# Performance work log

Measured on AMD Instinct MI355X. Metric: run time of the kernel, lower is better.

## Reference

```python
import jax, jax.numpy as jnp
import numpy as np

NUM_CLASSES = 7
CLASS_WEIGHT = 1.0
BOX_WEIGHT = 1.0


def _linear_sum_assignment(cost):
    """Exact Hungarian via shortest augmenting paths (Jonker-Volgenant style).
    Matches scipy.optimize.linear_sum_assignment for rectangular matrices:
    returns (row_ind, col_ind) of length min(n, m), row_ind sorted ascending."""
    C = np.asarray(cost, dtype=np.float64)
    transposed = C.shape[0] > C.shape[1]
    if transposed:
        C = C.T
    n, m = C.shape  # n <= m
    u = np.zeros(n + 1)
    v = np.zeros(m + 1)
    p = np.zeros(m + 1, dtype=np.int64)    # p[j]: row matched to col j (1-based); 0 = free
    way = np.zeros(m + 1, dtype=np.int64)
    for i in range(1, n + 1):
        p[0] = i
        j0 = 0
        minv = np.full(m + 1, np.inf)
        used = np.zeros(m + 1, dtype=bool)
        while True:
            used[j0] = True
            i0 = p[j0]
            cur = C[i0 - 1] - u[i0] - v[1:]
            free = ~used[1:]
            better = free & (cur < minv[1:])
            minv[1:][better] = cur[better]
            way[1:][better] = j0
            masked = np.where(free, minv[1:], np.inf)
            j0n = int(np.argmin(masked)) + 1
            delta = masked[j0n - 1]
            uj = np.nonzero(used)[0]
            u[p[uj]] += delta
            v[uj] -= delta
            minv[1:][free] -= delta
            j0 = j0n
            if p[j0] == 0:
                break
        while j0 != 0:   # augment along alternating path
            j1 = way[j0]
            p[j0] = p[j1]
            j0 = j1
    cols = np.nonzero(p[1:] > 0)[0]
    rows = p[1:][cols] - 1
    if transposed:
        rows, cols = cols, rows
    order = np.argsort(rows)
    return rows[order], cols[order]


def _cost_matrices(pred_logits, pred_boxes, gt_labels, gt_boxes):
    """Batched cost: class_weight * (-log_softmax gathered at gt labels) + box_weight * L1 cdist on xyz."""
    B, Q, _ = pred_logits.shape
    M = gt_labels.shape[1]
    log_probs = jax.nn.log_softmax(pred_logits, axis=-1)                       # (B,Q,C)
    idx = jnp.broadcast_to(gt_labels[:, None, :], (B, Q, M))
    class_cost = -jnp.take_along_axis(log_probs, idx, axis=2)                  # (B,Q,M)
    box_cost = jnp.sum(jnp.abs(pred_boxes[:, :, None, :3] - gt_boxes[:, None, :, :3]), axis=-1)  # (B,Q,M)
    return CLASS_WEIGHT * class_cost + BOX_WEIGHT * box_cost


def _matched_loss(pred_logits, pred_boxes, gt_labels, gt_boxes, rows, cols):
    B = pred_logits.shape[0]
    bidx = jnp.arange(B)[:, None]
    ml = pred_logits[bidx, rows]          # (B,M,C) matched logits
    mb = pred_boxes[bidx, rows]           # (B,M,7) matched boxes
    gl = gt_labels[bidx, cols]            # (B,M)
    gb = gt_boxes[bidx, cols]             # (B,M,7)
    logp = jax.nn.log_softmax(ml, axis=-1)
    ce = -jnp.mean(jnp.take_along_axis(logp, gl[..., None], axis=-1)[..., 0], axis=1)  # (B,)
    l1 = jnp.mean(jnp.abs(mb - gb), axis=(1, 2))                                       # (B,)
    return jnp.mean(CLASS_WEIGHT * ce + BOX_WEIGHT * l1)


def setup_inputs() -> dict:
    key = jax.random.key(0)
    k1, k2, k3, k4 = jax.random.split(key, 4)
    B, Q, M = 128, 900, 100
    return {
        'pred_logits': jax.random.normal(k1, (B, Q, NUM_CLASSES), dtype=jnp.float32),
        'pred_boxes': jax.random.normal(k2, (B, Q, 7), dtype=jnp.float32),
        'gt_labels': jax.random.randint(k3, (B, M), 0, NUM_CLASSES, dtype=jnp.int32),
        'gt_boxes': jax.random.normal(k4, (B, M, 7), dtype=jnp.float32),
    }


def reference(pred_logits, pred_boxes, gt_labels, gt_boxes):
    B = pred_logits.shape[0]
    M = gt_labels.shape[1]
    # Assignment is done on detached costs (host-side), matching the original module.
    cost = np.asarray(_cost_matrices(pred_logits, pred_boxes, gt_labels, gt_boxes))
    rows = np.zeros((B, M), dtype=np.int64)
    cols = np.zeros((B, M), dtype=np.int64)
    for b in range(B):
        r, c = _linear_sum_assignment(cost[b])
        rows[b], cols[b] = r, c
    return _matched_loss(pred_logits, pred_boxes, gt_labels, gt_boxes,
                         jnp.asarray(rows), jnp.asarray(cols))
```

## Files before the change

kernel.cpp:

```cpp
#include <hip/hip_runtime.h>
#include <math.h>


#define NQ   900
#define NG   100
#define NC   7
#define CPL  15
#define ROUNDS 10
#define INFF __builtin_inff()

__device__ __forceinline__ float readlane_f(float x, int l) {
  return __int_as_float(__builtin_amdgcn_readlane(__float_as_int(x), l));
}
template<int CTRL>
__device__ __forceinline__ float dpp_min_step(float x) {
  int y = __builtin_amdgcn_update_dpp(__float_as_int(x), __float_as_int(x),
                                      CTRL, 0xf, 0xf, false);
  return fminf(x, __int_as_float(y));
}
__device__ __forceinline__ float wave_min_b(float x) {
  x = dpp_min_step<0x111>(x);
  x = dpp_min_step<0x112>(x);
  x = dpp_min_step<0x114>(x);
  x = dpp_min_step<0x118>(x);
  x = dpp_min_step<0x142>(x);
  x = dpp_min_step<0x143>(x);
  return __int_as_float(__builtin_amdgcn_readlane(__float_as_int(x), 63));
}
template<int CTRL>
__device__ __forceinline__ void dpp_min2_step(float &a, float &b) {
  const int INFI = 0x7f800000;
  float a2 = __int_as_float(__builtin_amdgcn_update_dpp(
      INFI, __float_as_int(a), CTRL, 0xf, 0xf, false));
  float b2 = __int_as_float(__builtin_amdgcn_update_dpp(
      INFI, __float_as_int(b), CTRL, 0xf, 0xf, false));
  float lo = fminf(a, a2);
  float hi = fmaxf(a, a2);
  b = fminf(hi, fminf(b, b2));
  a = lo;
}
__device__ __forceinline__ void wave_min2_b(float m1, float m2,
                                            float &o1, float &o2) {
  dpp_min2_step<0x111>(m1, m2);
  dpp_min2_step<0x112>(m1, m2);
  dpp_min2_step<0x114>(m1, m2);
  dpp_min2_step<0x118>(m1, m2);
  dpp_min2_step<0x142>(m1, m2);
  dpp_min2_step<0x143>(m1, m2);
  o1 = readlane_f(m1, 63);
  o2 = readlane_f(m2, 63);
}
template<int CTRL>
__device__ __forceinline__ float dpp_add_step(float x) {
  int y = __builtin_amdgcn_update_dpp(0, __float_as_int(x),
                                      CTRL, 0xf, 0xf, true);
  return x + __int_as_float(y);
}
__device__ __forceinline__ float wave_sum_b(float x) {
  x = dpp_add_step<0x111>(x);
  x = dpp_add_step<0x112>(x);
  x = dpp_add_step<0x114>(x);
  x = dpp_add_step<0x118>(x);
  x = dpp_add_step<0x142>(x);
  x = dpp_add_step<0x143>(x);
  return __int_as_float(__builtin_amdgcn_readlane(__float_as_int(x), 63));
}
__device__ __forceinline__ void gl_lds16(const float* g, float* lds_base) {
  __builtin_amdgcn_global_load_lds(
      (const __attribute__((address_space(1))) unsigned int*)g,
      (__attribute__((address_space(3))) unsigned int*)lds_base, 16, 0, 0);
}
__device__ __forceinline__ float sel7v(float a0,float a1,float a2,float a3,
                                       float a4,float a5,float a6,int lab){
  float r = a0;
  r = lab==1 ? a1 : r;  r = lab==2 ? a2 : r;  r = lab==3 ? a3 : r;
  r = lab==4 ? a4 : r;  r = lab==5 ? a5 : r;  r = lab==6 ? a6 : r;
  return r;
}

__global__ __launch_bounds__(256, 1) void hungarian_fused_kernel(
    const float* __restrict__ logits, const float* __restrict__ pboxes,
    const int* __restrict__ glabels, const float* __restrict__ gboxes,
    float* __restrict__ out, float inv_B)
{
  const int b = blockIdx.x, tid = threadIdx.x;
  const int lane = tid & 63, w = tid >> 6;

  __shared__ __align__(16) float s_raw[NQ * NC];
  __shared__ __align__(16) float s_nlpT[NC * 1024];
  __shared__ __align__(16) float s_pb[960 * NC];
  __shared__ __align__(16) float s_gb[NG * NC];
  __shared__ __align__(16) int   s_glab[NG];
  __shared__ float s_u[NG + 1];
  __shared__ float s_v[CPL * 64];
  __shared__ int   s_p[NQ];
  __shared__ unsigned s_bid[NQ];
  __shared__ int   s_rmatch[NG];
  __shared__ float s_bm1[NG], s_bm2[NG];
  __shared__ int   s_bc[NG];
  __shared__ unsigned long long s_fm[2];
  __shared__ float s_f1v[NG]; __shared__ int s_f1c[NG];
  __shared__ float s_f2v[NG]; __shared__ int s_f2c[NG];
  __shared__ int   s_mlist[128];

  {
    const float* Lg = logits + (size_t)b * NQ * NC;
    const float* Pg = pboxes + (size_t)b * NQ * NC;
    const float* Gg = gboxes + (size_t)b * NG * NC;
    const int*   Bg = glabels + (size_t)b * NG;
    #pragma unroll
    for (int t = 0; t < 7; t++) {
      int i = (t << 8) + tid;
      if (i < (NQ * NC) / 4) {
        gl_lds16(Lg + i * 4, s_raw + ((t << 8) + (w << 6)) * 4);
        gl_lds16(Pg + i * 4, s_pb  + ((t << 8) + (w << 6)) * 4);
      }
    }
    if (tid < (NG * NC) / 4) gl_lds16(Gg + tid * 4, s_gb + (w << 6) * 4);
    if (tid < NG / 4) gl_lds16((const float*)Bg + tid * 4, (float*)s_glab);
    for (int i = tid; i < (960 - NQ) * NC; i += 256) s_pb[NQ * NC + i] = 0.f;
    for (int c = tid; c < NQ; c += 256) { s_p[c] = 0x7fffffff; s_bid[c] = 0xFFFFFFFFu; }
    for (int i = tid; i < CPL * 64; i += 256) s_v[i] = 0.f;
    if (tid == 0) s_u[0] = 0.f;
  }
  __syncthreads();

  for (int i = tid; i < 960; i += 256) {
    int L = i & 63, t = i >> 6;
    int q = L * CPL + t;
    float o[NC];
    if (q < NQ) {
      float x[NC];
      #pragma unroll
      for (int c = 0; c < NC; c++) x[c] = s_raw[q * NC + c];
      float mx = x[0];
      #pragma unroll
      for (int c = 1; c < NC; c++) mx = fmaxf(mx, x[c]);
      float tt[NC]; float se = 0.f;
      #pragma unroll
      for (int c = 0; c < NC; c++) { tt[c] = x[c] - mx; se += __expf(tt[c]); }
      float lg = __logf(se);
      #pragma unroll
      for (int c = 0; c < NC; c++) o[c] = lg - tt[c];
    } else {
      #pragma unroll
      for (int c = 0; c < NC; c++) o[c] = INFF;
    }
    #pragma unroll
    for (int c = 0; c < NC; c++) s_nlpT[c * 1024 + t * 64 + L] = o[c];
  }
  __syncthreads();

  const bool lval = (lane < NQ / CPL);
  float cpx[CPL], cpy[CPL], cpz[CPL];
  #pragma unroll
  for (int t = 0; t < CPL; t++) {
    int c = lane * CPL + t;
    cpx[t]=s_pb[c*NC+0]; cpy[t]=s_pb[c*NC+1]; cpz[t]=s_pb[c*NC+2];
  }

  for (int rl = 0; rl < 25; rl++) {
    int r = w * 25 + rl;
    int lab = s_glab[r];
    float gx = s_gb[r*NC+0], gy = s_gb[r*NC+1], gz = s_gb[r*NC+2];
    float m1 = INFF; int c1t = 0;
    #pragma unroll
    for (int t = 0; t < CPL; t++) {
      float nl = s_nlpT[lab*1024 + t*64 + lane];
      float bs = fabsf(cpx[t]-gx)+fabsf(cpy[t]-gy)+fabsf(cpz[t]-gz);
      float cost = nl + bs;
      bool lt1 = cost < m1;
      c1t = lt1 ? t : c1t;
      m1 = fminf(m1, cost);
    }
    float w1 = wave_min_b(m1);
    unsigned long long mk = __ballot(m1 == w1);
    int src = (int)__builtin_ctzll(mk);
    int col = __builtin_amdgcn_readlane(lane * CPL + c1t, src);
    if (lane == 0) {
      s_u[r + 1] = w1;
      s_bc[r] = col;
      atomicMin(&s_p[col], r + 1);
    }
  }
  __syncthreads();
  for (int c = tid; c < NQ; c += 256) if (s_p[c] == 0x7fffffff) s_p[c] = 0;
  if (tid < NG) {
    int c = s_bc[tid];
    s_rmatch[tid] = (s_p[c] == tid + 1) ? c + 1 : 0;
  }
  __syncthreads();

  for (int round = 0; round < ROUNDS; round++) {
    if (w == 0) {
      unsigned long long m = __ballot(s_rmatch[lane] == 0);
      if (lane == 0) s_fm[0] = m;
    } else if (w == 1) {
      unsigned long long m = __ballot((lane < NG - 64) && s_rmatch[64 + lane] == 0);
      if (lane == 0) s_fm[1] = m;
    }
    __syncthreads();
    const unsigned long long fm0r = s_fm[0], fm1r = s_fm[1];
    if ((fm0r | fm1r) == 0) break;
    float vreg[CPL];
    #pragma unroll
    for (int t = 0; t < CPL; t++) vreg[t] = s_v[t*64 + lane];
    {
      unsigned long long mm0 = fm0r, mm1 = fm1r;
      int idx = 0;
      while (mm0 | mm1) {
        int r;
        if (mm0) { int b2 = (int)__builtin_ctzll(mm0); mm0 &= mm0 - 1; r = b2; }
        else     { int b2 = (int)__builtin_ctzll(mm1); mm1 &= mm1 - 1; r = 64 + b2; }
        if ((idx++ & 3) != w) continue;
        int lab = s_glab[r];
        float gx = s_gb[r*NC+0], gy = s_gb[r*NC+1], gz = s_gb[r*NC+2];
        float m1 = INFF, m2 = INFF; int c1t = 0;
        #pragma unroll
        for (int t = 0; t < CPL; t++) {
          float nl = s_nlpT[lab*1024 + t*64 + lane];
          float bs = fabsf(cpx[t]-gx)+fabsf(cpy[t]-gy)+fabsf(cpz[t]-gz);
          float cost = (nl + bs) - vreg[t];
          bool lt1 = cost < m1;
          m2 = lt1 ? m1 : fminf(m2, cost);
          c1t = lt1 ? t : c1t;
          m1 = fminf(m1, cost);
        }
        float w1, w2;
        wave_min2_b(m1, m2, w1, w2);
        unsigned long long mk = __ballot(m1 == w1);
        int src = (int)__builtin_ctzll(mk);
        int col1 = __builtin_amdgcn_readlane(lane * CPL + c1t, src);
        if (lane == 0) {
          s_bm1[r] = w1; s_bm2[r] = w2; s_bc[r] = col1;
          atomicMin(&s_bid[col1],
                    (__float_as_uint(w1) & 0xFFFFFF80u) | (unsigned)(r + 1));
        }
      }
    }
    __syncthreads();
    if (tid < NG) {
      bool wasfree = (tid < 64) ? ((fm0r >> tid) & 1ull)
                                : ((fm1r >> (tid - 64)) & 1ull);
      if (wasfree) {
        int c = s_bc[tid];
        if ((s_bid[c] & 0x7Fu) == (unsigned)(tid + 1)) {
          int dold = s_p[c];
          s_p[c] = tid + 1;
          s_rmatch[tid] = c + 1;
          if (dold > 0) s_rmatch[dold - 1] = 0;
          s_u[tid + 1] = s_bm2[tid];
          s_v[(c % CPL) * 64 + (c / CPL)] -= (s_bm2[tid] - s_bm1[tid]);
        }
      }
    }
    __syncthreads();
    if (tid < NG) {
      bool wasfree = (tid < 64) ? ((fm0r >> tid) & 1ull)
                                : ((fm1r >> (tid - 64)) & 1ull);
      if (wasfree) s_bid[s_bc[tid]] = 0xFFFFFFFFu;
    }
  }
  __syncthreads();

  if (w == 0) {
    unsigned long long m = __ballot(s_rmatch[lane] == 0);
    if (lane == 0) s_fm[0] = m;
  } else if (w == 1) {
    unsigned long long m = __ballot((lane < NG - 64) && s_rmatch[64 + lane] == 0);
    if (lane == 0) s_fm[1] = m;
  }
  __syncthreads();
  const unsigned long long ff0 = s_fm[0], ff1 = s_fm[1];
  const int nfinal = __popcll(ff0) + __popcll(ff1);
  if (nfinal > 0) {
    float vreg[CPL];
    #pragma unroll
    for (int t = 0; t < CPL; t++) vreg[t] = s_v[t*64 + lane];
    unsigned long long mm0 = ff0, mm1 = ff1;
    int idx = 0;
    while (mm0 | mm1) {
      int r;
      if (mm0) { int b2 = (int)__builtin_ctzll(mm0); mm0 &= mm0 - 1; r = b2; }
      else     { int b2 = (int)__builtin_ctzll(mm1); mm1 &= mm1 - 1; r = 64 + b2; }
      if ((idx++ & 3) != w) continue;
      int lab = s_glab[r];
      float gx = s_gb[r*NC+0], gy = s_gb[r*NC+1], gz = s_gb[r*NC+2];
      float m1 = INFF;
      #pragma unroll
      for (int t = 0; t < CPL; t++) {
        float nl = s_nlpT[lab*1024 + t*64 + lane];
        float bs = fabsf(cpx[t]-gx)+fabsf(cpy[t]-gy)+fabsf(cpz[t]-gz);
        m1 = fminf(m1, (nl + bs) - vreg[t]);
      }
      float w1 = wave_min_b(m1);
      if (lane == 0) s_u[r + 1] = w1;
    }
    __syncthreads();
  }

  if (nfinal > 0) {
  unsigned fmask = 0;
  if (lval) {
    #pragma unroll
    for (int t = 0; t < CPL; t++)
      if (s_p[lane * CPL + t] == 0) fmask |= (1u << t);
  }

  auto top2row = [&](int lab, float gx, float gy, float gz,
                     float &o1v, int &o1c, float &o2v, int &o2c) {
    float m1 = INFF, m2 = INFF; int c1 = 0, c2 = 0;
    #pragma unroll
    for (int t = 0; t < CPL; t++) {
      float nl = s_nlpT[lab*1024 + t*64 + lane];
      float bs = fabsf(cpx[t]-gx)+fabsf(cpy[t]-gy)+fabsf(cpz[t]-gz);
      float cost = nl + bs;
      cost = ((fmask >> t) & 1u) ? cost : INFF;
      bool lt1 = cost < m1;
      bool lt2 = cost < m2;
      c2 = lt1 ? c1 : (lt2 ? t : c2);
      m2 = lt1 ? m1 : fminf(m2, cost);
      c1 = lt1 ? t : c1;
      m1 = fminf(m1, cost);
    }
    float w1 = wave_min_b(m1);
    unsigned long long mk = __ballot(m1 == w1);
    int src = (int)__builtin_ctzll(mk);
    int col1 = __builtin_amdgcn_readlane(lane * CPL + c1, src);
    float alt = (lane == src) ? m2 : m1;
    int  altc = (lane == src) ? c2 : c1;
    float w2 = wave_min_b(alt);
    unsigned long long mk2 = __ballot(alt == w2);
    int src2 = (int)__builtin_ctzll(mk2);
    int col2 = __builtin_amdgcn_readlane(lane * CPL + altc, src2);
    o1v = w1; o1c = col1; o2v = w2; o2c = col2;
  };

  for (int rl = 0; rl < 25; rl++) {
    int r = w * 25 + rl;
    int lab = s_glab[r];
    float gx = s_gb[r*NC+0], gy = s_gb[r*NC+1], gz = s_gb[r*NC+2];
    float v1, v2; int cc1, cc2;
    top2row(lab, gx, gy, gz, v1, cc1, v2, cc2);
    if (lane == 0) {
      s_f1v[r] = v1; s_f1c[r] = cc1; s_f2v[r] = v2; s_f2c[r] = cc2;
    }
  }
  __syncthreads();
  if (w != 0) return;

  volatile float* vu = s_u;

  const bool r1ok = (lane < NG - 64);
  int   rlab0 = s_glab[lane];
  float rgx0 = s_gb[lane*NC+0], rgy0 = s_gb[lane*NC+1], rgz0 = s_gb[lane*NC+2];
  int   rlab1 = 0; float rgx1=0.f, rgy1=0.f, rgz1=0.f;
  if (r1ok) {
    int r = 64 + lane;
    rlab1 = s_glab[r];
    rgx1 = s_gb[r*NC+0]; rgy1 = s_gb[r*NC+1]; rgz1 = s_gb[r*NC+2];
  }
  float ru0 = vu[lane + 1];
  float ru1 = r1ok ? vu[lane + 65] : 0.f;
  float rf1v0 = s_f1v[lane];       int rf1c0 = s_f1c[lane];
  float rf2v0 = s_f2v[lane];       int rf2c0 = s_f2c[lane];
  float rf1v1 = r1ok ? s_f1v[64+lane] : INFF; int rf1c1 = r1ok ? s_f1c[64+lane] : -1;
  float rf2v1 = r1ok ? s_f2v[64+lane] : INFF; int rf2c1 = r1ok ? s_f2c[64+lane] : -1;

  unsigned long long fm0 = ff0;
  unsigned long long fm1 = ff1;

  int NM = 0;
  #pragma unroll
  for (int t = 0; t < CPL; t++) {
    int c = lane * CPL + t;
    bool has = lval && (s_p[c] > 0);
    unsigned long long m = __ballot(has);
    int pos = NM + (int)__popcll(m & ((1ull << lane) - 1ull));
    if (has) s_mlist[pos] = c;
    NM += (int)__popcll(m);
  }

  int   mcol[2]  = {-1,-1};
  int   mprow[2] = {0,0};
  float mpu[2]   = {0.f,0.f};
  float mv[2]    = {0.f,0.f};
  float mx[2]={0,0}, my[2]={0,0}, mz[2]={0,0};
  float mn0[2],mn1[2],mn2[2],mn3[2],mn4[2],mn5[2],mn6[2];
  #pragma unroll
  for (int k = 0; k < 2; k++) { mn0[k]=0;mn1[k]=0;mn2[k]=0;mn3[k]=0;mn4[k]=0;mn5[k]=0;mn6[k]=0; }
  #pragma unroll
  for (int k = 0; k < 2; k++) {
    int s = lane + (k << 6);
    if (s < NM) {
      int c = s_mlist[s];
      int cq = c / CPL, ct = c - cq * CPL;
      mcol[k] = c;
      mx[k] = s_pb[c*NC+0]; my[k] = s_pb[c*NC+1]; mz[k] = s_pb[c*NC+2];
      mn0[k] = s_nlpT[0*1024 + ct*64 + cq];
      mn1[k] = s_nlpT[1*1024 + ct*64 + cq];
      mn2[k] = s_nlpT[2*1024 + ct*64 + cq];
      mn3[k] = s_nlpT[3*1024 + ct*64 + cq];
      mn4[k] = s_nlpT[4*1024 + ct*64 + cq];
      mn5[k] = s_nlpT[5*1024 + ct*64 + cq];
      mn6[k] = s_nlpT[6*1024 + ct*64 + cq];
      mprow[k] = s_p[c];
      mpu[k] = vu[mprow[k]];
      mv[k] = s_v[ct * 64 + cq];
    }
  }

  float dsl[2]; int wsl[2];

  for (int half = 0; half < 2; half++) {
    unsigned long long fm = half ? fm1 : fm0;
    while (fm) {
      int bit = (int)__builtin_ctzll(fm);
      fm &= fm - 1;
      int rfree = bit + (half ? 65 : 1);
      dsl[0] = INFF; dsl[1] = INFF; wsl[0] = 0; wsl[1] = 0;
      unsigned usedm = 0;
      float bfv = INFF; int bfc = -1, bfprev = 0;
      int i0 = rfree;
      int ro0 = rfree - 1;
      float u_i0 = readlane_f((ro0 >> 6) ? ru1 : ru0, ro0 & 63);
      int j0p = 0;
      float minVal = 0.f;
      int jf = -1, jfprev = 0;

      for (int it = 0; it < 128; it++) {
        int ro = i0 - 1, rown = ro & 63, rs = ro >> 6;
        int   lab = __builtin_amdgcn_readlane(rs ? rlab1 : rlab0, rown);
        float gx = readlane_f(rs ? rgx1 : rgx0, rown);
        float gy = readlane_f(rs ? rgy1 : rgy0, rown);
        float gz = readlane_f(rs ? rgz1 : rgz0, rown);
        float hs = minVal - u_i0;
        float f1v = readlane_f(rs ? rf1v1 : rf1v0, rown);
        int   f1c = __builtin_amdgcn_readlane(rs ? rf1c1 : rf1c0, rown);
        float cbf = f1v + hs;
        if (cbf < bfv) { bfv = cbf; bfc = f1c; bfprev = j0p; }
        float lb = INFF; int bk = 0;
        #pragma unroll
        for (int k = 0; k < 2; k++) {
          bool gate = ((lane + (k << 6)) < NM) && !((usedm >> k) & 1u);
          float nl = sel7v(mn0[k],mn1[k],mn2[k],mn3[k],mn4[k],mn5[k],mn6[k],lab);
          float bs = fabsf(mx[k]-gx)+fabsf(my[k]-gy)+fabsf(mz[k]-gz);
          float rr = ((nl + bs) + hs) - mv[k];
          bool imp = gate && (rr < dsl[k]);
          dsl[k] = imp ? rr : dsl[k];
          wsl[k] = imp ? j0p : wsl[k];
          float cand = gate ? dsl[k] : INFF;
          bool bt = cand < lb;
          bk = bt ? k : bk;
          lb = fminf(lb, cand);
        }
        float dm = wave_min_b(lb);
        if (bfv <= dm) { minVal = bfv; jf = bfc; jfprev = bfprev; break; }
        unsigned long long msk = __ballot(lb == dm);
        int src = (int)__builtin_ctzll(msk);
        int spk = __builtin_amdgcn_readlane((bk << 6) | lane, src);
        minVal = dm;
        int so = spk & 63, sk = spk >> 6;
        usedm |= (lane == so) ? (1u << sk) : 0u;
        i0  = __builtin_amdgcn_readlane(sk ? mprow[1] : mprow[0], so);
        u_i0 = readlane_f(sk ? mpu[1] : mpu[0], so);
        j0p = spk + 1;
      }
      if (jf < 0) { jf = bfc; jfprev = bfprev; minVal = bfv; }

      if (lane == 0) vu[rfree] += minVal;
      #pragma unroll
      for (int k = 0; k < 2; k++) {
        if ((usedm >> k) & 1u) {
          float a = minVal - dsl[k];
          mv[k] -= a;
          vu[mprow[k]] += a;
        }
      }
      __threadfence_block();

      int pred = jfprev;
      int nr;
      if (pred == 0) nr = rfree;
      else {
        int s = pred - 1;
        nr = __builtin_amdgcn_readlane((s >> 6) ? mprow[1] : mprow[0], s & 63);
      }
      if (lane == 0) s_p[jf] = nr;
      {
        int cq = jf / CPL, ct = jf - cq * CPL;
        float nx = s_pb[jf*NC+0], ny = s_pb[jf*NC+1], nz = s_pb[jf*NC+2];
        float a0 = s_nlpT[0*1024 + ct*64 + cq];
        float a1 = s_nlpT[1*1024 + ct*64 + cq];
        float a2 = s_nlpT[2*1024 + ct*64 + cq];
        float a3 = s_nlpT[3*1024 + ct*64 + cq];
        float a4 = s_nlpT[4*1024 + ct*64 + cq];
        float a5 = s_nlpT[5*1024 + ct*64 + cq];
        float a6 = s_nlpT[6*1024 + ct*64 + cq];
        int kk = NM >> 6;
        if (lane == (NM & 63) && NM < 128) {
          if (kk == 0) {
            mcol[0]=jf; mx[0]=nx; my[0]=ny; mz[0]=nz; mprow[0]=nr; mv[0]=0.f;
            mn0[0]=a0;mn1[0]=a1;mn2[0]=a2;mn3[0]=a3;mn4[0]=a4;mn5[0]=a5;mn6[0]=a6;
          } else {
            mcol[1]=jf; mx[1]=nx; my[1]=ny; mz[1]=nz; mprow[1]=nr; mv[1]=0.f;
            mn0[1]=a0;mn1[1]=a1;mn2[1]=a2;mn3[1]=a3;mn4[1]=a4;mn5[1]=a5;mn6[1]=a6;
          }
        }
        NM++;
      }
      while (pred) {
        int s = pred - 1, so = s & 63, sk = s >> 6;
        int np = __builtin_amdgcn_readlane(sk ? wsl[1] : wsl[0], so);
        int nr2;
        if (np == 0) nr2 = rfree;
        else {
          int s2 = np - 1;
          nr2 = __builtin_amdgcn_readlane((s2 >> 6) ? mprow[1] : mprow[0], s2 & 63);
        }
        int sc = __builtin_amdgcn_readlane(sk ? mcol[1] : mcol[0], so);
        if (lane == so) { if (sk) mprow[1] = nr2; else mprow[0] = nr2; }
        if (lane == 0) s_p[sc] = nr2;
        pred = np;
      }
      __threadfence_block();

      ru0 = vu[lane + 1];
      if (r1ok) ru1 = vu[lane + 65];
      #pragma unroll
      for (int k = 0; k < 2; k++)
        if ((lane + (k << 6)) < NM) mpu[k] = vu[mprow[k]];

      if (lane == (jf / CPL)) fmask &= ~(1u << (jf - (jf / CPL) * CPL));
      if (rf1c0 == jf) { rf1v0 = rf2v0; rf1c0 = rf2c0; rf2c0 = -1; rf2v0 = INFF; }
      else if (rf2c0 == jf) { rf2c0 = -1; rf2v0 = INFF; }
      if (rf1c1 == jf) { rf1v1 = rf2v1; rf1c1 = rf2c1; rf2c1 = -1; rf2v1 = INFF; }
      else if (rf2c1 == jf) { rf2c1 = -1; rf2v1 = INFF; }
      unsigned long long need0 = __ballot(rf1c0 < 0);
      unsigned long long need1 = __ballot(r1ok && (rf1c1 < 0));
      while (need0) {
        int rb = (int)__builtin_ctzll(need0); need0 &= need0 - 1;
        int lab = __builtin_amdgcn_readlane(rlab0, rb);
        float gx = readlane_f(rgx0, rb), gy = readlane_f(rgy0, rb), gz = readlane_f(rgz0, rb);
        float v1, v2; int cc1, cc2;
        top2row(lab, gx, gy, gz, v1, cc1, v2, cc2);
        if (lane == rb) { rf1v0=v1; rf1c0=cc1; rf2v0=v2; rf2c0=cc2; }
      }
      while (need1) {
        int rb = (int)__builtin_ctzll(need1); need1 &= need1 - 1;
        int lab = __builtin_amdgcn_readlane(rlab1, rb);
        float gx = readlane_f(rgx1, rb), gy = readlane_f(rgy1, rb), gz = readlane_f(rgz1, rb);
        float v1, v2; int cc1, cc2;
        top2row(lab, gx, gy, gz, v1, cc1, v2, cc2);
        if (lane == rb) { rf1v1=v1; rf1c1=cc1; rf2v1=v2; rf2c1=cc2; }
      }
    }
  }
  }

  if (w != 0) return;
  {
    float ce = 0.f, l1 = 0.f;
    if (lval) {
      #pragma unroll
      for (int t = 0; t < CPL; t++) {
        int c = lane * CPL + t;
        int pr = s_p[c];
        if (pr > 0) {
          int g = pr - 1;
          int lg = s_glab[g];
          ce += s_nlpT[lg*1024 + t*64 + lane];
          float s = 0.f;
          #pragma unroll
          for (int d7 = 0; d7 < 7; d7++) s += fabsf(s_pb[c*NC+d7] - s_gb[g*NC+d7]);
          l1 += s;
        }
      }
    }
    float tot = ce * (1.f / NG) + l1 * (1.f / (NG * 7.f));
    tot = wave_sum_b(tot);
    if (lane == 0) atomicAdd(out, tot * inv_B);
  }
}

extern "C" void kernel_launch(void* const* d_in, const int* in_sizes, int n_in,
                              void* d_out, int out_size, void* d_ws, size_t ws_size,
                              hipStream_t stream) {
  const float* logits  = (const float*)d_in[0];
  const float* pboxes  = (const float*)d_in[1];
  const int*   glabels = (const int*)d_in[2];
  const float* gboxes  = (const float*)d_in[3];
  float* out = (float*)d_out;
  const int B = in_sizes[0] / (NQ * NC);

  hungarian_fused_kernel<<<dim3(B), dim3(256), 0, stream>>>(
      logits, pboxes, glabels, gboxes, out, 1.0f / (float)B);
}
```

Before: 128.3 us.

## Fuse argmin into DPP reductions and add greedy matching pass before JV

Replaces the wave-min followed by ballot/ctz/readlane with DPP reductions that carry the column index alongside the value, for both single and top-2 reductions. After the final dual-update pass it also computes each free row's best column and greedily assigns uncontested free columns, shrinking the set of rows that need serial augmenting-path search. This trades some extra DPP ops and syncs for fewer serial JV iterations. Tie-breaking among equal minima may differ from the lowest-lane rule used before.

New measurement: 129.3 us. Within noise of the previous version (+0.7%).

```diff
diff --git a/kernel.cpp b/kernel.cpp
--- a/kernel.cpp
+++ b/kernel.cpp
@@ -12,44 +12,56 @@
 __device__ __forceinline__ float readlane_f(float x, int l) {
   return __int_as_float(__builtin_amdgcn_readlane(__float_as_int(x), l));
 }
+
 template<int CTRL>
-__device__ __forceinline__ float dpp_min_step(float x) {
-  int y = __builtin_amdgcn_update_dpp(__float_as_int(x), __float_as_int(x),
-                                      CTRL, 0xf, 0xf, false);
-  return fminf(x, __int_as_float(y));
-}
-__device__ __forceinline__ float wave_min_b(float x) {
-  x = dpp_min_step<0x111>(x);
-  x = dpp_min_step<0x112>(x);
-  x = dpp_min_step<0x114>(x);
-  x = dpp_min_step<0x118>(x);
-  x = dpp_min_step<0x142>(x);
-  x = dpp_min_step<0x143>(x);
-  return __int_as_float(__builtin_amdgcn_readlane(__float_as_int(x), 63));
-}
+__device__ __forceinline__ void dpp_amin_step(float &v, int &ix) {
+  float v2 = __int_as_float(__builtin_amdgcn_update_dpp(
+      __float_as_int(v), __float_as_int(v), CTRL, 0xf, 0xf, false));
+  int i2 = __builtin_amdgcn_update_dpp(ix, ix, CTRL, 0xf, 0xf, false);
+  ix = (v2 < v) ? i2 : ix;
+  v  = fminf(v, v2);
+}
+__device__ __forceinline__ void wave_amin_b(float v, int ix, float &ov, int &oi) {
+  dpp_amin_step<0x111>(v, ix);
+  dpp_amin_step<0x112>(v, ix);
+  dpp_amin_step<0x114>(v, ix);
+  dpp_amin_step<0x118>(v, ix);
+  dpp_amin_step<0x142>(v, ix);
+  dpp_amin_step<0x143>(v, ix);
+  ov = readlane_f(v, 63);
+  oi = __builtin_amdgcn_readlane(ix, 63);
+}
+
 template<int CTRL>
-__device__ __forceinline__ void dpp_min2_step(float &a, float &b) {
+__device__ __forceinline__ void dpp_amin2_step(float &a, int &ia, float &b, int &ib) {
   const int INFI = 0x7f800000;
   float a2 = __int_as_float(__builtin_amdgcn_update_dpp(
       INFI, __float_as_int(a), CTRL, 0xf, 0xf, false));
   float b2 = __int_as_float(__builtin_amdgcn_update_dpp(
       INFI, __float_as_int(b), CTRL, 0xf, 0xf, false));
-  float lo = fminf(a, a2);
-  float hi = fmaxf(a, a2);
-  b = fminf(hi, fminf(b, b2));
-  a = lo;
-}
-__device__ __forceinline__ void wave_min2_b(float m1, float m2,
-                                            float &o1, float &o2) {
-  dpp_min2_step<0x111>(m1, m2);
-  dpp_min2_step<0x112>(m1, m2);
-  dpp_min2_step<0x114>(m1, m2);
-  dpp_min2_step<0x118>(m1, m2);
-  dpp_min2_step<0x142>(m1, m2);
-  dpp_min2_step<0x143>(m1, m2);
-  o1 = readlane_f(m1, 63);
-  o2 = readlane_f(m2, 63);
-}
+  int ia2 = __builtin_amdgcn_update_dpp(0, ia, CTRL, 0xf, 0xf, false);
+  int ib2 = __builtin_amdgcn_update_dpp(0, ib, CTRL, 0xf, 0xf, false);
+  bool sw = a2 < a;
+  float hi = sw ? a  : a2;  int ihi = sw ? ia  : ia2;
+  float lo = sw ? a2 : a;   int ilo = sw ? ia2 : ia;
+  bool t1 = b2 < b;
+  float bb = t1 ? b2 : b;   int ibb = t1 ? ib2 : ib;
+  bool t2 = hi < bb;
+  b = t2 ? hi : bb;         ib = t2 ? ihi : ibb;
+  a = lo; ia = ilo;
+}
+__device__ __forceinline__ void wave_amin2_b(float a, int ia, float b, int ib,
+    float &o1, int &oc1, float &o2, int &oc2) {
+  dpp_amin2_step<0x111>(a, ia, b, ib);
+  dpp_amin2_step<0x112>(a, ia, b, ib);
+  dpp_amin2_step<0x114>(a, ia, b, ib);
+  dpp_amin2_step<0x118>(a, ia, b, ib);
+  dpp_amin2_step<0x142>(a, ia, b, ib);
+  dpp_amin2_step<0x143>(a, ia, b, ib);
+  o1 = readlane_f(a, 63); oc1 = __builtin_amdgcn_readlane(ia, 63);
+  o2 = readlane_f(b, 63); oc2 = __builtin_amdgcn_readlane(ib, 63);
+}
+
 template<int CTRL>
 __device__ __forceinline__ float dpp_add_step(float x) {
   int y = __builtin_amdgcn_update_dpp(0, __float_as_int(x),
@@ -173,10 +185,8 @@
       c1t = lt1 ? t : c1t;
       m1 = fminf(m1, cost);
     }
-    float w1 = wave_min_b(m1);
-    unsigned long long mk = __ballot(m1 == w1);
-    int src = (int)__builtin_ctzll(mk);
-    int col = __builtin_amdgcn_readlane(lane * CPL + c1t, src);
+    float w1; int col;
+    wave_amin_b(m1, lane * CPL + c1t, w1, col);
     if (lane == 0) {
       s_u[r + 1] = w1;
       s_bc[r] = col;
@@ -226,11 +236,8 @@
           c1t = lt1 ? t : c1t;
           m1 = fminf(m1, cost);
         }
-        float w1, w2;
-        wave_min2_b(m1, m2, w1, w2);
-        unsigned long long mk = __ballot(m1 == w1);
-        int src = (int)__builtin_ctzll(mk);
-        int col1 = __builtin_amdgcn_readlane(lane * CPL + c1t, src);
+        float w1, w2; int col1, dumc;
+        wave_amin2_b(m1, lane * CPL + c1t, m2, 0, w1, col1, w2, dumc);
         if (lane == 0) {
           s_bm1[r] = w1; s_bm2[r] = w2; s_bc[r] = col1;
           atomicMin(&s_bid[col1],
@@ -273,6 +280,7 @@
   __syncthreads();
   const unsigned long long ff0 = s_fm[0], ff1 = s_fm[1];
   const int nfinal = __popcll(ff0) + __popcll(ff1);
+
   if (nfinal > 0) {
     float vreg[CPL];
     #pragma unroll
@@ -286,20 +294,56 @@
       if ((idx++ & 3) != w) continue;
       int lab = s_glab[r];
       float gx = s_gb[r*NC+0], gy = s_gb[r*NC+1], gz = s_gb[r*NC+2];
-      float m1 = INFF;
+      float m1 = INFF; int c1t = 0;
       #pragma unroll
       for (int t = 0; t < CPL; t++) {
         float nl = s_nlpT[lab*1024 + t*64 + lane];
         float bs = fabsf(cpx[t]-gx)+fabsf(cpy[t]-gy)+fabsf(cpz[t]-gz);
-        m1 = fminf(m1, (nl + bs) - vreg[t]);
-      }
-      float w1 = wave_min_b(m1);
-      if (lane == 0) s_u[r + 1] = w1;
+        float cost = (nl + bs) - vreg[t];
+        bool lt1 = cost < m1;
+        c1t = lt1 ? t : c1t;
+        m1 = fminf(m1, cost);
+      }
+      float w1; int col;
+      wave_amin_b(m1, lane * CPL + c1t, w1, col);
+      if (lane == 0) { s_u[r + 1] = w1; s_bc[r] = col; }
     }
     __syncthreads();
-  }
-
-  if (nfinal > 0) {
+    if (tid < NG) {
+      bool wasfree = (tid < 64) ? ((ff0 >> tid) & 1ull)
+                                : ((ff1 >> (tid - 64)) & 1ull);
+      if (wasfree) {
+        int c = s_bc[tid];
+        if (s_p[c] == 0) atomicMin(&s_bid[c], (unsigned)tid);
+      }
+    }
+    __syncthreads();
+    if (tid < NG) {
+      bool wasfree = (tid < 64) ? ((ff0 >> tid) & 1ull)
+                                : ((ff1 >> (tid - 64)) & 1ull);
+      if (wasfree) {
+        int c = s_bc[tid];
+        if (s_p[c] == 0 && s_bid[c] == (unsigned)tid) {
+          s_p[c] = tid + 1;
+          s_rmatch[tid] = c + 1;
+        }
+      }
+    }
+    __syncthreads();
+    if (w == 0) {
+      unsigned long long m = __ballot(s_rmatch[lane] == 0);
+      if (lane == 0) s_fm[0] = m;
+    } else if (w == 1) {
+      unsigned long long m = __ballot((lane < NG - 64) && s_rmatch[64 + lane] == 0);
+      if (lane == 0) s_fm[1] = m;
+    }
+    __syncthreads();
+  }
+
+  const unsigned long long gg0 = s_fm[0], gg1 = s_fm[1];
+  const int nf2 = __popcll(gg0) + __popcll(gg1);
+
+  if (nf2 > 0) {
   unsigned fmask = 0;
   if (lval) {
     #pragma unroll
@@ -323,17 +367,7 @@
       c1 = lt1 ? t : c1;
       m1 = fminf(m1, cost);
     }
-    float w1 = wave_min_b(m1);
-    unsigned long long mk = __ballot(m1 == w1);
-    int src = (int)__builtin_ctzll(mk);
-    int col1 = __builtin_amdgcn_readlane(lane * CPL + c1, src);
-    float alt = (lane == src) ? m2 : m1;
-    int  altc = (lane == src) ? c2 : c1;
-    float w2 = wave_min_b(alt);
-    unsigned long long mk2 = __ballot(alt == w2);
-    int src2 = (int)__builtin_ctzll(mk2);
-    int col2 = __builtin_amdgcn_readlane(lane * CPL + altc, src2);
-    o1v = w1; o1c = col1; o2v = w2; o2c = col2;
+    wave_amin2_b(m1, lane * CPL + c1, m2, lane * CPL + c2, o1v, o1c, o2v, o2c);
   };
 
   for (int rl = 0; rl < 25; rl++) {
@@ -367,8 +401,8 @@
   float rf1v1 = r1ok ? s_f1v[64+lane] : INFF; int rf1c1 = r1ok ? s_f1c[64+lane] : -1;
   float rf2v1 = r1ok ? s_f2v[64+lane] : INFF; int rf2c1 = r1ok ? s_f2c[64+lane] : -1;
 
-  unsigned long long fm0 = ff0;
-  unsigned long long fm1 = ff1;
+  unsigned long long fm0 = gg0;
+  unsigned long long fm1 = gg1;
 
   int NM = 0;
   #pragma unroll
@@ -454,11 +488,9 @@
           bk = bt ? k : bk;
           lb = fminf(lb, cand);
         }
-        float dm = wave_min_b(lb);
+        float dm; int spk;
+        wave_amin_b(lb, (bk << 6) | lane, dm, spk);
         if (bfv <= dm) { minVal = bfv; jf = bfc; jfprev = bfprev; break; }
-        unsigned long long msk = __ballot(lb == dm);
-        int src = (int)__builtin_ctzll(msk);
-        int spk = __builtin_amdgcn_readlane((bk << 6) | lane, src);
         minVal = dm;
         int so = spk & 63, sk = spk >> 6;
         usedm |= (lane == so) ? (1u << sk) : 0u;
```
